# Optimization experiments

Measured on AMD Instinct MI355X. Metric: run time of the kernel, lower is better.

The kernel has to match this reference:

```python
import jax, jax.numpy as jnp
import numpy as np

HID = 64   # hid_dim // 2 inside pocket_att_net2
H = 8      # n_heads


def _dist_mask(d):
    """get_mask: 8 distance bands, each carrying 1/d inside its band, else 0.
    band i (i=0..6): i < d <= i+3 ; band 7: d > 7.  Output [B, 8, Nl, Np]."""
    safe = jnp.where(d > 0, d, 1.0)
    inv = jnp.where(d > 0, 1.0 / safe, 0.0)
    bands = []
    for i in range(8):
        if i < 7:
            m = (d > float(i)) & (d <= float(i + 3))
        else:
            m = d > 7.0
        bands.append(jnp.where(m, inv, 0.0))
    return jnp.stack(bands, axis=1)


def setup_inputs() -> dict:
    key = jax.random.key(0)
    ks = jax.random.split(key, 20)
    B, Nl, Np = 16, 256, 2048
    s = 0.05
    inp = {
        "ligand": jax.random.normal(ks[0], (B, Nl, HID), jnp.float32),
        "prot":   jax.random.normal(ks[1], (B, Np, HID), jnp.float32),
        "dist":   jax.random.uniform(ks[2], (B, Nl, Np), jnp.float32) * 10.0,
        # projection weights (jax convention: x @ W + b)
        "w_l1": jax.random.normal(ks[3], (HID, HID * H), jnp.float32) * s,
        "b_l1": jnp.zeros((HID * H,), jnp.float32),
        "w_l2": jax.random.normal(ks[4], (HID, HID * H), jnp.float32) * s,
        "b_l2": jnp.zeros((HID * H,), jnp.float32),
        "w_p1": jax.random.normal(ks[5], (HID, HID * H), jnp.float32) * s,
        "b_p1": jnp.zeros((HID * H,), jnp.float32),
        "w_p2": jax.random.normal(ks[6], (HID, HID * H), jnp.float32) * s,
        "b_p2": jnp.zeros((HID * H,), jnp.float32),
        "fc11_w": jax.random.normal(ks[7], (HID * H, HID), jnp.float32) * s,
        "fc11_b": jnp.zeros((HID,), jnp.float32),
        "fc12_w": jax.random.normal(ks[8], (2 * HID, HID), jnp.float32) * s,
        "fc12_b": jnp.zeros((HID,), jnp.float32),
        "fc21_w": jax.random.normal(ks[9], (HID * H, HID), jnp.float32) * s,
        "fc21_b": jnp.zeros((HID,), jnp.float32),
        "fc22_w": jax.random.normal(ks[10], (2 * HID, HID), jnp.float32) * s,
        "fc22_b": jnp.zeros((HID,), jnp.float32),
    }
    return inp


def _proj(x, w, b):
    B, N, _ = x.shape
    h = jax.nn.relu(x @ w + b)                      # [B, N, H*HID]
    return h.reshape(B, N, H, HID).transpose(0, 2, 1, 3)  # [B, H, N, HID]


def reference(ligand, prot, dist, w_l1, b_l1, w_l2, b_l2, w_p1, b_p1, w_p2, b_p2,
              fc11_w, fc11_b, fc12_w, fc12_b, fc21_w, fc21_b, fc22_w, fc22_b):
    B, Nl, _ = ligand.shape
    Np = prot.shape[1]
    inter = _dist_mask(dist)                        # [B, H, Nl, Np]

    l1 = _proj(ligand, w_l1, b_l1)
    l2 = _proj(ligand, w_l2, b_l2)
    p1 = _proj(prot, w_p1, b_p1)
    p2 = _proj(prot, w_p2, b_p2)

    scale = jnp.sqrt(jnp.float32(HID))
    energy = jnp.einsum('bhld,bhpd->bhlp', l1, p1) / scale
    att = jax.nn.softmax(energy * inter, axis=-1)   # dropout = identity (eval)

    l3 = jnp.einsum('bhlp,bhpd->bhld', att, p2)
    l3 = l3.transpose(0, 2, 1, 3).reshape(B, Nl, H * HID)
    l3 = jnp.concatenate([l3 @ fc11_w + fc11_b, ligand], axis=2)
    l3 = jax.nn.relu(l3 @ fc12_w + fc12_b)          # [B, Nl, HID]

    p3 = jnp.einsum('bhlp,bhld->bhpd', att, l2)
    p3 = p3.transpose(0, 2, 1, 3).reshape(B, Np, H * HID)
    p3 = jnp.concatenate([p3 @ fc21_w + fc21_b, prot], axis=2)
    p3 = jax.nn.relu(p3 @ fc22_w + fc22_b)          # [B, Np, HID]

    return jnp.concatenate([l3, p3], axis=1)        # [B, Nl+Np, HID]
```

## Files before the change

### kernel.cpp

```cpp
#include <hip/hip_runtime.h>
#include <hip/hip_bf16.h>

typedef _Float16 f16x8 __attribute__((ext_vector_type(8)));
typedef _Float16 f16x4 __attribute__((ext_vector_type(4)));
typedef float f32x4 __attribute__((ext_vector_type(4)));

#define B_   16
#define NL   256
#define NP   2048
#define NH   8
#define PSPLIT 4
#define PCHUNK (NP / PSPLIT)

static __device__ __forceinline__ f32x4 mfma16(f16x8 a, f16x8 b, f32x4 c) {
  return __builtin_amdgcn_mfma_f32_16x16x32_f16(a, b, c, 0, 0, 0);
}

__global__ __launch_bounds__(256) void proj_kernel(
    const float* __restrict__ x, const float* __restrict__ W, const float* __restrict__ bias,
    _Float16* __restrict__ outA, _Float16* __restrict__ outB, int N, int mode)
{
  __shared__ float xt[64][68];
  const int t = threadIdx.x;
  const int n0 = blockIdx.x * 64;
  const int h  = blockIdx.y;
  const int b  = blockIdx.z;

  const float* xp = x + ((size_t)b * N + n0) * 64;
#pragma unroll
  for (int i = 0; i < 4; ++i) {
    int flat = (i * 256 + t) * 4;
    f32x4 v = *(const f32x4*)(xp + flat);
    *(f32x4*)&xt[flat >> 6][flat & 63] = v;
  }
  __syncthreads();

  const int nb = (t >> 4) * 4;
  const int db = (t & 15) * 4;

  float acc[4][4];
#pragma unroll
  for (int i = 0; i < 4; ++i)
#pragma unroll
    for (int j = 0; j < 4; ++j) acc[i][j] = bias[h * 64 + db + j];

  const float* wp = W + h * 64 + db;
#pragma unroll 8
  for (int k = 0; k < 64; ++k) {
    f32x4 wq = *(const f32x4*)(wp + (size_t)k * 512);
    float a0 = xt[nb + 0][k], a1 = xt[nb + 1][k], a2 = xt[nb + 2][k], a3 = xt[nb + 3][k];
#pragma unroll
    for (int j = 0; j < 4; ++j) {
      acc[0][j] += a0 * wq[j];
      acc[1][j] += a1 * wq[j];
      acc[2][j] += a2 * wq[j];
      acc[3][j] += a3 * wq[j];
    }
  }

  if (mode == 0) {
#pragma unroll
    for (int i = 0; i < 4; ++i) {
      f16x4 hv, lv;
#pragma unroll
      for (int j = 0; j < 4; ++j) {
        float v = fmaxf(acc[i][j], 0.f);
        _Float16 hi = (_Float16)v;
        hv[j] = hi;
        lv[j] = (_Float16)((v - (float)hi) * 2048.0f);
      }
      size_t idx = (((size_t)b * NH + h) * N + n0 + nb + i) * 64 + db;
      *(f16x4*)(outA + idx) = hv;
      *(f16x4*)(outB + idx) = lv;
    }
  } else {
#pragma unroll
    for (int j = 0; j < 4; ++j) {
      f16x4 tv;
#pragma unroll
      for (int i = 0; i < 4; ++i) tv[i] = (_Float16)fmaxf(acc[i][j], 0.f);
      size_t idx = (((size_t)b * NH + h) * 64 + db + j) * N + n0 + nb;
      *(f16x4*)(outA + idx) = tv;
    }
  }
}

__global__ __launch_bounds__(512, 4) void flash_l3_kernel(
    const _Float16* __restrict__ l1h, const _Float16* __restrict__ l1l,
    const _Float16* __restrict__ p1h, const _Float16* __restrict__ p1l,
    const _Float16* __restrict__ p2t, const float* __restrict__ dist,
    float* __restrict__ l3p, float* __restrict__ mpart, float* __restrict__ spart)
{
  const int sb = blockIdx.x;
  const int sp = sb & (PSPLIT - 1);
  const int b  = sb >> 2;
  const int lt = blockIdx.y;
  const int t  = threadIdx.x;
  const int h    = t >> 6;
  const int lane = t & 63;
  const int g = lane >> 4, c = lane & 15;
  const int l0 = lt * 16;
  const int bh = b * NH + h;
  const int NT = PCHUNK / 64;

  __shared__ float distT[2][64][20];
  __shared__ _Float16 P[NH][16][72];

  const size_t l1off = ((size_t)bh * NL + l0 + c) * 64;
  f16x8 aLh[2], aLl[2];
  aLh[0] = *(const f16x8*)(l1h + l1off + g * 8);
  aLh[1] = *(const f16x8*)(l1h + l1off + 32 + g * 8);
  aLl[0] = *(const f16x8*)(l1l + l1off + g * 8);
  aLl[1] = *(const f16x8*)(l1l + l1off + 32 + g * 8);

  f32x4 accO[4];
#pragma unroll
  for (int dt = 0; dt < 4; ++dt) accO[dt] = (f32x4){0.f, 0.f, 0.f, 0.f};
  float m_r[4] = {-INFINITY, -INFINITY, -INFINITY, -INFINITY};
  float s_r[4] = {0.f, 0.f, 0.f, 0.f};

  const float* dbase = dist + ((size_t)b * NL + l0) * NP + sp * PCHUNK;
  const _Float16* p1hb = p1h + ((size_t)bh * NP + sp * PCHUNK) * 64;
  const _Float16* p1lb = p1l + ((size_t)bh * NP + sp * PCHUNK) * 64;
  const _Float16* p2tb = p2t + (size_t)bh * 64 * NP + sp * PCHUNK;
  const float fh = (float)h, fh3 = fh + 3.0f;

  const int dl_p = t & 63;
  const int dl_l = t >> 6;

  {
    float dv0 = dbase[(size_t)dl_l * NP + dl_p];
    float dv1 = dbase[(size_t)(dl_l + 8) * NP + dl_p];
    distT[0][dl_p][dl_l]     = dv0;
    distT[0][dl_p][dl_l + 8] = dv1;
  }

  for (int it = 0; it < NT; ++it) {
    const int P0 = it * 64;
    const int cur = it & 1;
    __syncthreads();

    float nv0 = 0.f, nv1 = 0.f;
    if (it + 1 < NT) {
      nv0 = dbase[(size_t)dl_l * NP + P0 + 64 + dl_p];
      nv1 = dbase[(size_t)(dl_l + 8) * NP + P0 + 64 + dl_p];
    }

    f16x8 v0[4], v1[4];
#pragma unroll
    for (int dt = 0; dt < 4; ++dt) {
      const _Float16* vp = p2tb + (size_t)(dt * 16 + c) * NP + P0 + g * 8;
      v0[dt] = *(const f16x8*)(vp);
      v1[dt] = *(const f16x8*)(vp + 32);
    }

    float mev[4][4];
    float cmax[4] = {-INFINITY, -INFINITY, -INFINITY, -INFINITY};
#pragma unroll
    for (int s = 0; s < 4; ++s) {
      const _Float16* ph = p1hb + (size_t)(P0 + s * 16 + c) * 64;
      const _Float16* pl = p1lb + (size_t)(P0 + s * 16 + c) * 64;
      f16x8 bh0 = *(const f16x8*)(ph + g * 8);
      f16x8 bh1 = *(const f16x8*)(ph + 32 + g * 8);
      f16x8 bl0 = *(const f16x8*)(pl + g * 8);
      f16x8 bl1 = *(const f16x8*)(pl + 32 + g * 8);
      f32x4 e  = (f32x4){0.f, 0.f, 0.f, 0.f};
      f32x4 ec = (f32x4){0.f, 0.f, 0.f, 0.f};
      __builtin_amdgcn_s_setprio(1);
      e  = mfma16(aLh[0], bh0, e);  e  = mfma16(aLh[1], bh1, e);
      ec = mfma16(aLh[0], bl0, ec); ec = mfma16(aLh[1], bl1, ec);
      ec = mfma16(aLl[0], bh0, ec); ec = mfma16(aLl[1], bh1, ec);
      __builtin_amdgcn_s_setprio(0);
      f32x4 dq = *(const f32x4*)&distT[cur][s * 16 + c][g * 4];
#pragma unroll
      for (int r = 0; r < 4; ++r) {
        float dv = dq[r];
        float ev = (e[r] + ec[r] * (1.0f / 2048.0f)) * 0.125f;
        bool cond = (h < 7) ? (dv > fh && dv <= fh3) : (dv > 7.0f);
        float m = cond ? ev * __builtin_amdgcn_rcpf(dv) : 0.0f;
        mev[s][r] = m;
        cmax[r] = fmaxf(cmax[r], m);
      }
    }
#pragma unroll
    for (int mask = 1; mask < 16; mask <<= 1)
#pragma unroll
      for (int r = 0; r < 4; ++r)
        cmax[r] = fmaxf(cmax[r], __shfl_xor(cmax[r], mask, 64));

#pragma unroll
    for (int r = 0; r < 4; ++r) {
      float mn  = fmaxf(m_r[r], cmax[r]);
      float fac = __expf(m_r[r] - mn);
      m_r[r] = mn;
      float ss = 0.f;
#pragma unroll
      for (int s = 0; s < 4; ++s) {
        float pv = __expf(mev[s][r] - mn);
        ss += pv;
        P[h][g * 4 + r][s * 16 + c] = (_Float16)pv;
      }
      s_r[r] = s_r[r] * fac + ss;
#pragma unroll
      for (int dt = 0; dt < 4; ++dt) accO[dt][r] *= fac;
    }
    {
      f16x8 aP0 = *(const f16x8*)&P[h][c][g * 8];
      f16x8 aP1 = *(const f16x8*)&P[h][c][32 + g * 8];
      __builtin_amdgcn_s_setprio(1);
#pragma unroll
      for (int dt = 0; dt < 4; ++dt) accO[dt] = mfma16(aP0, v0[dt], accO[dt]);
#pragma unroll
      for (int dt = 0; dt < 4; ++dt) accO[dt] = mfma16(aP1, v1[dt], accO[dt]);
      __builtin_amdgcn_s_setprio(0);
    }
    if (it + 1 < NT) {
      distT[cur ^ 1][dl_p][dl_l]     = nv0;
      distT[cur ^ 1][dl_p][dl_l + 8] = nv1;
    }
  }

#pragma unroll
  for (int mask = 1; mask < 16; mask <<= 1)
#pragma unroll
    for (int r = 0; r < 4; ++r) s_r[r] += __shfl_xor(s_r[r], mask, 64);

  float* lp = l3p + (size_t)sp * B_ * NL * 512;
#pragma unroll
  for (int dt = 0; dt < 4; ++dt)
#pragma unroll
    for (int r = 0; r < 4; ++r)
      lp[((size_t)b * NL + l0 + g * 4 + r) * 512 + h * 64 + dt * 16 + c] = accO[dt][r];

  if (c == 0) {
#pragma unroll
    for (int r = 0; r < 4; ++r) {
      size_t li = (size_t)sp * B_ * NH * NL + (size_t)bh * NL + l0 + g * 4 + r;
      mpart[li] = m_r[r];
      spart[li] = s_r[r];
    }
  }
}

__global__ __launch_bounds__(256) void merge_l3_kernel(
    const float* __restrict__ l3p, const float* __restrict__ mpart, const float* __restrict__ spart,
    float* __restrict__ l3c, float* __restrict__ mrow, float* __restrict__ rsrow)
{
  const int row = blockIdx.x * 4 + (threadIdx.x >> 6);
  const int d   = threadIdx.x & 63;
  const int l   = row & (NL - 1);
  const int bh  = row >> 8;
  const int b = bh >> 3, h = bh & 7;
  const size_t srow = (size_t)B_ * NH * NL;

  float mi[PSPLIT], si[PSPLIT];
  float M = -INFINITY;
#pragma unroll
  for (int i = 0; i < PSPLIT; ++i) {
    mi[i] = mpart[(size_t)i * srow + row];
    si[i] = spart[(size_t)i * srow + row];
    M = fmaxf(M, mi[i]);
  }
  const float* lp = l3p + ((size_t)b * NL + l) * 512 + h * 64 + d;
  float S = 0.f, o = 0.f;
#pragma unroll
  for (int i = 0; i < PSPLIT; ++i) {
    float w = __expf(mi[i] - M);
    S += si[i] * w;
    o += lp[(size_t)i * B_ * NL * 512] * w;
  }
  float rs = 1.0f / S;
  l3c[((size_t)b * NL + l) * 512 + h * 64 + d] = o * rs;
  if (d == 0) { mrow[row] = M; rsrow[row] = rs; }
}

__global__ __launch_bounds__(512, 4) void p3_kernel(
    const _Float16* __restrict__ p1h, const _Float16* __restrict__ p1l,
    const _Float16* __restrict__ l1h, const _Float16* __restrict__ l1l,
    const _Float16* __restrict__ l2t, const float* __restrict__ dist,
    const float* __restrict__ mrow, const float* __restrict__ rsrow,
    float* __restrict__ p3c)
{
  const int b  = blockIdx.x;
  const int pt = blockIdx.y;
  const int t  = threadIdx.x;
  const int h    = t >> 6;
  const int lane = t & 63;
  const int g = lane >> 4, c = lane & 15;
  const int p0 = pt * 16;
  const int bh = b * NH + h;
  const int NT = NL / 32;

  __shared__ float distT[2][32][20];
  __shared__ _Float16 PT[NH][16][40];

  const size_t poff = ((size_t)bh * NP + p0 + c) * 64;
  f16x8 aPh[2], aPl[2];
  aPh[0] = *(const f16x8*)(p1h + poff + g * 8);
  aPh[1] = *(const f16x8*)(p1h + poff + 32 + g * 8);
  aPl[0] = *(const f16x8*)(p1l + poff + g * 8);
  aPl[1] = *(const f16x8*)(p1l + poff + 32 + g * 8);

  f32x4 acc[4];
#pragma unroll
  for (int dt = 0; dt < 4; ++dt) acc[dt] = (f32x4){0.f, 0.f, 0.f, 0.f};

  const float* db_ = dist + (size_t)b * NL * NP + p0;
  const _Float16* l1hb = l1h + (size_t)bh * NL * 64;
  const _Float16* l1lb = l1l + (size_t)bh * NL * 64;
  const _Float16* l2tb = l2t + (size_t)bh * 64 * NL;
  const float* mb = mrow + (size_t)bh * NL;
  const float* rb = rsrow + (size_t)bh * NL;
  const float fh = (float)h, fh3 = fh + 3.0f;

  const int dl_l = t >> 4;
  const int dl_p = t & 15;

  distT[0][dl_l][dl_p] = db_[(size_t)dl_l * NP + dl_p];

  for (int it = 0; it < NT; ++it) {
    const int lc = it * 32;
    const int cur = it & 1;
    __syncthreads();

    float nv = 0.f;
    if (it + 1 < NT)
      nv = db_[(size_t)(lc + 32 + dl_l) * NP + dl_p];

    f16x8 bV[4];
#pragma unroll
    for (int dt = 0; dt < 4; ++dt)
      bV[dt] = *(const f16x8*)(l2tb + (size_t)(dt * 16 + c) * NL + lc + g * 8);

#pragma unroll
    for (int s = 0; s < 2; ++s) {
      const int l = lc + s * 16 + c;
      const _Float16* lhp = l1hb + (size_t)l * 64;
      const _Float16* llp = l1lb + (size_t)l * 64;
      f16x8 bh0 = *(const f16x8*)(lhp + g * 8);
      f16x8 bh1 = *(const f16x8*)(lhp + 32 + g * 8);
      f16x8 bl0 = *(const f16x8*)(llp + g * 8);
      f16x8 bl1 = *(const f16x8*)(llp + 32 + g * 8);
      f32x4 e  = (f32x4){0.f, 0.f, 0.f, 0.f};
      f32x4 ec = (f32x4){0.f, 0.f, 0.f, 0.f};
      __builtin_amdgcn_s_setprio(1);
      e  = mfma16(aPh[0], bh0, e);  e  = mfma16(aPh[1], bh1, e);
      ec = mfma16(aPh[0], bl0, ec); ec = mfma16(aPh[1], bl1, ec);
      ec = mfma16(aPl[0], bh0, ec); ec = mfma16(aPl[1], bh1, ec);
      __builtin_amdgcn_s_setprio(0);
      float ml = mb[l], rl = rb[l];
      f32x4 dq = *(const f32x4*)&distT[cur][s * 16 + c][g * 4];
#pragma unroll
      for (int r = 0; r < 4; ++r) {
        float ev = (e[r] + ec[r] * (1.0f / 2048.0f)) * 0.125f;
        float dvv = dq[r];
        bool cond = (h < 7) ? (dvv > fh && dvv <= fh3) : (dvv > 7.0f);
        float m = cond ? ev * __builtin_amdgcn_rcpf(dvv) : 0.0f;
        float att = __expf(m - ml) * rl;
        PT[h][g * 4 + r][s * 16 + c] = (_Float16)att;
      }
    }
    {
      f16x8 aA = *(const f16x8*)&PT[h][c][g * 8];
      __builtin_amdgcn_s_setprio(1);
#pragma unroll
      for (int dt = 0; dt < 4; ++dt) acc[dt] = mfma16(aA, bV[dt], acc[dt]);
      __builtin_amdgcn_s_setprio(0);
    }
    if (it + 1 < NT)
      distT[cur ^ 1][dl_l][dl_p] = nv;
  }

#pragma unroll
  for (int dt = 0; dt < 4; ++dt)
#pragma unroll
    for (int r = 0; r < 4; ++r)
      p3c[((size_t)b * NP + p0 + g * 4 + r) * 512 + h * 64 + dt * 16 + c] = acc[dt][r];
}

__global__ __launch_bounds__(256) void fc_out_kernel(
    const float* __restrict__ x3c, const float* __restrict__ xbase,
    const float* __restrict__ wA, const float* __restrict__ bA,
    const float* __restrict__ wB, const float* __restrict__ bB,
    float* __restrict__ out, int N, int out_off)
{
  __shared__ float xl[16][520];
  __shared__ float t1[16][68];
  __shared__ float xb[16][68];
  const int t = threadIdx.x;
  const int row0 = blockIdx.x * 16;

  const float* xp = x3c + (size_t)row0 * 512;
#pragma unroll
  for (int i = 0; i < 8; ++i) {
    int flat = (i * 256 + t) * 4;
    f32x4 v = *(const f32x4*)(xp + flat);
    *(f32x4*)&xl[flat >> 9][flat & 511] = v;
  }
  {
    const float* bp = xbase + (size_t)row0 * 64;
    int flat = t * 4;
    f32x4 v = *(const f32x4*)(bp + flat);
    *(f32x4*)&xb[flat >> 6][flat & 63] = v;
  }
  __syncthreads();

  const int r  = t >> 4;
  const int c4 = (t & 15) * 4;

  float acc[4];
#pragma unroll
  for (int j = 0; j < 4; ++j) acc[j] = bA[c4 + j];
  for (int k4 = 0; k4 < 128; ++k4) {
    f32x4 xq = *(const f32x4*)&xl[r][k4 * 4];
#pragma unroll
    for (int kk = 0; kk < 4; ++kk) {
      f32x4 wq = *(const f32x4*)(wA + (size_t)(k4 * 4 + kk) * 64 + c4);
#pragma unroll
      for (int j = 0; j < 4; ++j) acc[j] += xq[kk] * wq[j];
    }
  }
#pragma unroll
  for (int j = 0; j < 4; ++j) t1[r][c4 + j] = acc[j];
  __syncthreads();

  float a2[4];
#pragma unroll
  for (int j = 0; j < 4; ++j) a2[j] = bB[c4 + j];
  for (int k4 = 0; k4 < 32; ++k4) {
    f32x4 xq = (k4 < 16) ? *(const f32x4*)&t1[r][k4 * 4]
                         : *(const f32x4*)&xb[r][k4 * 4 - 64];
#pragma unroll
    for (int kk = 0; kk < 4; ++kk) {
      f32x4 wq = *(const f32x4*)(wB + (size_t)(k4 * 4 + kk) * 64 + c4);
#pragma unroll
      for (int j = 0; j < 4; ++j) a2[j] += xq[kk] * wq[j];
    }
  }
  const int row = row0 + r;
  const int b = row / N, n = row % N;
  f32x4 o;
#pragma unroll
  for (int j = 0; j < 4; ++j) o[j] = fmaxf(a2[j], 0.f);
  *(f32x4*)(out + (((size_t)b * (NL + NP)) + out_off + n) * 64 + c4) = o;
}

extern "C" void kernel_launch(void* const* d_in, const int* in_sizes, int n_in,
                              void* d_out, int out_size, void* d_ws, size_t ws_size,
                              hipStream_t stream)
{
  const float* ligand = (const float*)d_in[0];
  const float* prot   = (const float*)d_in[1];
  const float* dist   = (const float*)d_in[2];
  const float* w_l1   = (const float*)d_in[3];
  const float* b_l1   = (const float*)d_in[4];
  const float* w_l2   = (const float*)d_in[5];
  const float* b_l2   = (const float*)d_in[6];
  const float* w_p1   = (const float*)d_in[7];
  const float* b_p1   = (const float*)d_in[8];
  const float* w_p2   = (const float*)d_in[9];
  const float* b_p2   = (const float*)d_in[10];
  const float* fc11_w = (const float*)d_in[11];
  const float* fc11_b = (const float*)d_in[12];
  const float* fc12_w = (const float*)d_in[13];
  const float* fc12_b = (const float*)d_in[14];
  const float* fc21_w = (const float*)d_in[15];
  const float* fc21_b = (const float*)d_in[16];
  const float* fc22_w = (const float*)d_in[17];
  const float* fc22_b = (const float*)d_in[18];
  float* out = (float*)d_out;

  char* ws = (char*)d_ws;
  size_t off = 0;
  auto alloc = [&](size_t bytes) -> void* {
    void* p = ws + off;
    off += (bytes + 255) & ~(size_t)255;
    return p;
  };
  const size_t L1E = (size_t)B_ * NH * NL * 64;
  const size_t P1E = (size_t)B_ * NH * NP * 64;
  _Float16* l1h = (_Float16*)alloc(L1E * 2);
  _Float16* l1l = (_Float16*)alloc(L1E * 2);
  _Float16* p1h = (_Float16*)alloc(P1E * 2);
  _Float16* p1l = (_Float16*)alloc(P1E * 2);
  _Float16* l2t = (_Float16*)alloc(L1E * 2);
  _Float16* p2t = (_Float16*)alloc(P1E * 2);
  float* mrow  = (float*)alloc((size_t)B_ * NH * NL * 4);
  float* rsrow = (float*)alloc((size_t)B_ * NH * NL * 4);
  float* mpart = (float*)alloc((size_t)PSPLIT * B_ * NH * NL * 4);
  float* spart = (float*)alloc((size_t)PSPLIT * B_ * NH * NL * 4);
  float* l3c = (float*)alloc((size_t)B_ * NL * 512 * 4);
  float* p3c = (float*)alloc((size_t)B_ * NP * 512 * 4);
  float* l3p = p3c;

  proj_kernel<<<dim3(NL / 64, NH, B_), 256, 0, stream>>>(ligand, w_l1, b_l1, l1h, l1l, NL, 0);
  proj_kernel<<<dim3(NL / 64, NH, B_), 256, 0, stream>>>(ligand, w_l2, b_l2, l2t, nullptr, NL, 1);
  proj_kernel<<<dim3(NP / 64, NH, B_), 256, 0, stream>>>(prot, w_p1, b_p1, p1h, p1l, NP, 0);
  proj_kernel<<<dim3(NP / 64, NH, B_), 256, 0, stream>>>(prot, w_p2, b_p2, p2t, nullptr, NP, 1);

  flash_l3_kernel<<<dim3(PSPLIT * B_, NL / 16), 512, 0, stream>>>(
      l1h, l1l, p1h, p1l, p2t, dist, l3p, mpart, spart);
  merge_l3_kernel<<<(B_ * NH * NL) / 4, 256, 0, stream>>>(l3p, mpart, spart, l3c, mrow, rsrow);
  p3_kernel<<<dim3(B_, NP / 16), 512, 0, stream>>>(p1h, p1l, l1h, l1l, l2t, dist,
                                                   mrow, rsrow, p3c);

  fc_out_kernel<<<(B_ * NL) / 16, 256, 0, stream>>>(l3c, ligand, fc11_w, fc11_b,
                                                    fc12_w, fc12_b, out, NL, 0);
  fc_out_kernel<<<(B_ * NP) / 16, 256, 0, stream>>>(p3c, prot, fc21_w, fc21_b,
                                                    fc22_w, fc22_b, out, NP, NL);
}
```

Before: 870.5 us.

## Split attention heads across blocks and double P-axis split for occupancy

Both the flash l3 kernel and the p3 kernel now run 256-thread blocks that cover 4 heads each, with a grid z-dimension of 2 head groups. The flash kernel also splits the protein axis into 8 chunks instead of 4. V-operand loads move from the top of the loop to just before their MFMAs to cut live registers, and loop unrolling is disabled. The aim is more resident blocks and more parallel work. In exchange, each distance tile is now fetched by two blocks instead of one, and the transposed distT padding changes from 20 to 17, which replaces vector LDS reads with scalar ones.

```diff
diff --git a/kernel.cpp b/kernel.cpp
--- a/kernel.cpp
+++ b/kernel.cpp
@@ -9,7 +9,7 @@
 #define NL   256
 #define NP   2048
 #define NH   8
-#define PSPLIT 4
+#define PSPLIT 8
 #define PCHUNK (NP / PSPLIT)
 
 static __device__ __forceinline__ f32x4 mfma16(f16x8 a, f16x8 b, f32x4 c) {
@@ -85,7 +85,7 @@
   }
 }
 
-__global__ __launch_bounds__(512, 4) void flash_l3_kernel(
+__global__ __launch_bounds__(256) void flash_l3_kernel(
     const _Float16* __restrict__ l1h, const _Float16* __restrict__ l1l,
     const _Float16* __restrict__ p1h, const _Float16* __restrict__ p1l,
     const _Float16* __restrict__ p2t, const float* __restrict__ dist,
@@ -93,18 +93,20 @@
 {
   const int sb = blockIdx.x;
   const int sp = sb & (PSPLIT - 1);
-  const int b  = sb >> 2;
+  const int b  = sb >> 3;
   const int lt = blockIdx.y;
+  const int hg = blockIdx.z;
   const int t  = threadIdx.x;
-  const int h    = t >> 6;
+  const int w    = t >> 6;
+  const int h    = hg * 4 + w;
   const int lane = t & 63;
   const int g = lane >> 4, c = lane & 15;
   const int l0 = lt * 16;
   const int bh = b * NH + h;
   const int NT = PCHUNK / 64;
 
-  __shared__ float distT[2][64][20];
-  __shared__ _Float16 P[NH][16][72];
+  __shared__ float distT[2][64][17];
+  __shared__ _Float16 P[4][16][72];
 
   const size_t l1off = ((size_t)bh * NL + l0 + c) * 64;
   f16x8 aLh[2], aLl[2];
@@ -126,32 +128,22 @@
   const float fh = (float)h, fh3 = fh + 3.0f;
 
   const int dl_p = t & 63;
-  const int dl_l = t >> 6;
-
-  {
-    float dv0 = dbase[(size_t)dl_l * NP + dl_p];
-    float dv1 = dbase[(size_t)(dl_l + 8) * NP + dl_p];
-    distT[0][dl_p][dl_l]     = dv0;
-    distT[0][dl_p][dl_l + 8] = dv1;
-  }
-
+
+#pragma unroll
+  for (int i = 0; i < 4; ++i)
+    distT[0][dl_p][w * 4 + i] = dbase[(size_t)(w * 4 + i) * NP + dl_p];
+
+#pragma unroll 1
   for (int it = 0; it < NT; ++it) {
     const int P0 = it * 64;
     const int cur = it & 1;
     __syncthreads();
 
-    float nv0 = 0.f, nv1 = 0.f;
+    float nv[4];
     if (it + 1 < NT) {
-      nv0 = dbase[(size_t)dl_l * NP + P0 + 64 + dl_p];
-      nv1 = dbase[(size_t)(dl_l + 8) * NP + P0 + 64 + dl_p];
-    }
-
-    f16x8 v0[4], v1[4];
-#pragma unroll
-    for (int dt = 0; dt < 4; ++dt) {
-      const _Float16* vp = p2tb + (size_t)(dt * 16 + c) * NP + P0 + g * 8;
-      v0[dt] = *(const f16x8*)(vp);
-      v1[dt] = *(const f16x8*)(vp + 32);
+#pragma unroll
+      for (int i = 0; i < 4; ++i)
+        nv[i] = dbase[(size_t)(w * 4 + i) * NP + P0 + 64 + dl_p];
     }
 
     float mev[4][4];
@@ -171,10 +163,9 @@
       ec = mfma16(aLh[0], bl0, ec); ec = mfma16(aLh[1], bl1, ec);
       ec = mfma16(aLl[0], bh0, ec); ec = mfma16(aLl[1], bh1, ec);
       __builtin_amdgcn_s_setprio(0);
-      f32x4 dq = *(const f32x4*)&distT[cur][s * 16 + c][g * 4];
 #pragma unroll
       for (int r = 0; r < 4; ++r) {
-        float dv = dq[r];
+        float dv = distT[cur][s * 16 + c][g * 4 + r];
         float ev = (e[r] + ec[r] * (1.0f / 2048.0f)) * 0.125f;
         bool cond = (h < 7) ? (dv > fh && dv <= fh3) : (dv > 7.0f);
         float m = cond ? ev * __builtin_amdgcn_rcpf(dv) : 0.0f;
@@ -198,25 +189,27 @@
       for (int s = 0; s < 4; ++s) {
         float pv = __expf(mev[s][r] - mn);
         ss += pv;
-        P[h][g * 4 + r][s * 16 + c] = (_Float16)pv;
+        P[w][g * 4 + r][s * 16 + c] = (_Float16)pv;
       }
       s_r[r] = s_r[r] * fac + ss;
 #pragma unroll
       for (int dt = 0; dt < 4; ++dt) accO[dt][r] *= fac;
     }
-    {
-      f16x8 aP0 = *(const f16x8*)&P[h][c][g * 8];
-      f16x8 aP1 = *(const f16x8*)&P[h][c][32 + g * 8];
+#pragma unroll
+    for (int kk = 0; kk < 2; ++kk) {
+      f16x8 aP = *(const f16x8*)&P[w][c][kk * 32 + g * 8];
       __builtin_amdgcn_s_setprio(1);
 #pragma unroll
-      for (int dt = 0; dt < 4; ++dt) accO[dt] = mfma16(aP0, v0[dt], accO[dt]);
-#pragma unroll
-      for (int dt = 0; dt < 4; ++dt) accO[dt] = mfma16(aP1, v1[dt], accO[dt]);
+      for (int dt = 0; dt < 4; ++dt) {
+        f16x8 bV = *(const f16x8*)(p2tb + (size_t)(dt * 16 + c) * NP + P0 + kk * 32 + g * 8);
+        accO[dt] = mfma16(aP, bV, accO[dt]);
+      }
       __builtin_amdgcn_s_setprio(0);
     }
     if (it + 1 < NT) {
-      distT[cur ^ 1][dl_p][dl_l]     = nv0;
-      distT[cur ^ 1][dl_p][dl_l + 8] = nv1;
+#pragma unroll
+      for (int i = 0; i < 4; ++i)
+        distT[cur ^ 1][dl_p][w * 4 + i] = nv[i];
     }
   }
 
@@ -274,7 +267,7 @@
   if (d == 0) { mrow[row] = M; rsrow[row] = rs; }
 }
 
-__global__ __launch_bounds__(512, 4) void p3_kernel(
+__global__ __launch_bounds__(256) void p3_kernel(
     const _Float16* __restrict__ p1h, const _Float16* __restrict__ p1l,
     const _Float16* __restrict__ l1h, const _Float16* __restrict__ l1l,
     const _Float16* __restrict__ l2t, const float* __restrict__ dist,
@@ -283,8 +276,10 @@
 {
   const int b  = blockIdx.x;
   const int pt = blockIdx.y;
+  const int hg = blockIdx.z;
   const int t  = threadIdx.x;
-  const int h    = t >> 6;
+  const int w    = t >> 6;
+  const int h    = hg * 4 + w;
   const int lane = t & 63;
   const int g = lane >> 4, c = lane & 15;
   const int p0 = pt * 16;
@@ -292,7 +287,7 @@
   const int NT = NL / 32;
 
   __shared__ float distT[2][32][20];
-  __shared__ _Float16 PT[NH][16][40];
+  __shared__ _Float16 PT[4][16][40];
 
   const size_t poff = ((size_t)bh * NP + p0 + c) * 64;
   f16x8 aPh[2], aPl[2];
@@ -316,21 +311,22 @@
   const int dl_l = t >> 4;
   const int dl_p = t & 15;
 
-  distT[0][dl_l][dl_p] = db_[(size_t)dl_l * NP + dl_p];
-
+#pragma unroll
+  for (int i = 0; i < 2; ++i)
+    distT[0][dl_l + 16 * i][dl_p] = db_[(size_t)(dl_l + 16 * i) * NP + dl_p];
+
+#pragma unroll 1
   for (int it = 0; it < NT; ++it) {
     const int lc = it * 32;
     const int cur = it & 1;
     __syncthreads();
 
-    float nv = 0.f;
-    if (it + 1 < NT)
-      nv = db_[(size_t)(lc + 32 + dl_l) * NP + dl_p];
-
-    f16x8 bV[4];
-#pragma unroll
-    for (int dt = 0; dt < 4; ++dt)
-      bV[dt] = *(const f16x8*)(l2tb + (size_t)(dt * 16 + c) * NL + lc + g * 8);
+    float nv[2];
+    if (it + 1 < NT) {
+#pragma unroll
+      for (int i = 0; i < 2; ++i)
+        nv[i] = db_[(size_t)(lc + 32 + dl_l + 16 * i) * NP + dl_p];
+    }
 
 #pragma unroll
     for (int s = 0; s < 2; ++s) {
@@ -357,18 +353,24 @@
         bool cond = (h < 7) ? (dvv > fh && dvv <= fh3) : (dvv > 7.0f);
         float m = cond ? ev * __builtin_amdgcn_rcpf(dvv) : 0.0f;
         float att = __expf(m - ml) * rl;
-        PT[h][g * 4 + r][s * 16 + c] = (_Float16)att;
+        PT[w][g * 4 + r][s * 16 + c] = (_Float16)att;
       }
     }
     {
-      f16x8 aA = *(const f16x8*)&PT[h][c][g * 8];
+      f16x8 aA = *(const f16x8*)&PT[w][c][g * 8];
       __builtin_amdgcn_s_setprio(1);
 #pragma unroll
-      for (int dt = 0; dt < 4; ++dt) acc[dt] = mfma16(aA, bV[dt], acc[dt]);
+      for (int dt = 0; dt < 4; ++dt) {
+        f16x8 bV = *(const f16x8*)(l2tb + (size_t)(dt * 16 + c) * NL + lc + g * 8);
+        acc[dt] = mfma16(aA, bV, acc[dt]);
+      }
       __builtin_amdgcn_s_setprio(0);
     }
-    if (it + 1 < NT)
-      distT[cur ^ 1][dl_l][dl_p] = nv;
+    if (it + 1 < NT) {
+#pragma unroll
+      for (int i = 0; i < 2; ++i)
+        distT[cur ^ 1][dl_l + 16 * i][dl_p] = nv[i];
+    }
   }
 
 #pragma unroll
@@ -498,11 +500,11 @@
   proj_kernel<<<dim3(NP / 64, NH, B_), 256, 0, stream>>>(prot, w_p1, b_p1, p1h, p1l, NP, 0);
   proj_kernel<<<dim3(NP / 64, NH, B_), 256, 0, stream>>>(prot, w_p2, b_p2, p2t, nullptr, NP, 1);
 
-  flash_l3_kernel<<<dim3(PSPLIT * B_, NL / 16), 512, 0, stream>>>(
+  flash_l3_kernel<<<dim3(PSPLIT * B_, NL / 16, 2), 256, 0, stream>>>(
       l1h, l1l, p1h, p1l, p2t, dist, l3p, mpart, spart);
   merge_l3_kernel<<<(B_ * NH * NL) / 4, 256, 0, stream>>>(l3p, mpart, spart, l3c, mrow, rsrow);
-  p3_kernel<<<dim3(B_, NP / 16), 512, 0, stream>>>(p1h, p1l, l1h, l1l, l2t, dist,
-                                                   mrow, rsrow, p3c);
+  p3_kernel<<<dim3(B_, NP / 16, 2), 256, 0, stream>>>(p1h, p1l, l1h, l1l, l2t, dist,
+                                                      mrow, rsrow, p3c);
 
   fc_out_kernel<<<(B_ * NL) / 16, 256, 0, stream>>>(l3c, ligand, fc11_w, fc11_b,
                                                     fc12_w, fc12_b, out, NL, 0);
```

Result: faster. 799.1 us (-8.2%).
